# Optimization experiments

Hardware: AMD Instinct MI355X
Metric: run time of the kernel (lower is better)

Reference implementation:

```python
import jax, jax.numpy as jnp
import numpy as np
import math

B, S, D, H, L, DFF, NHEADS_OUT = 2, 1024, 1024, 16, 4, 4096, 3
DK = D // H
LN_EPS = 1e-5


def setup_inputs() -> dict:
    key = jax.random.key(0)
    ks = jax.random.split(key, 16)
    w = lambda k, shp: jax.random.normal(k, shp, dtype=jnp.float32) * 0.02
    return {
        "src": jax.random.normal(ks[0], (B, S, 1), dtype=jnp.float32),
        "emb_w": w(ks[1], (1, D)), "emb_b": jnp.zeros((D,), jnp.float32),
        "pe": w(ks[2], (S, D)),
        "Wq": w(ks[3], (L, D, D)), "bq": jnp.zeros((L, D), jnp.float32),
        "Wk": w(ks[4], (L, D, D)), "bk": jnp.zeros((L, D), jnp.float32),
        "Wv": w(ks[5], (L, D, D)), "bv": jnp.zeros((L, D), jnp.float32),
        "Wo": w(ks[6], (L, D, D)), "bo": jnp.zeros((L, D), jnp.float32),
        "fc1_w": w(ks[7], (L, D, DFF)), "fc1_b": jnp.zeros((L, DFF), jnp.float32),
        "fc2_w": w(ks[8], (L, DFF, D)), "fc2_b": jnp.zeros((L, D), jnp.float32),
        "ln1_g": jnp.ones((L, D), jnp.float32), "ln1_b": jnp.zeros((L, D), jnp.float32),
        "ln2_g": jnp.ones((L, D), jnp.float32), "ln2_b": jnp.zeros((L, D), jnp.float32),
        "hw1": w(ks[9], (NHEADS_OUT, D, D)), "hb1": jnp.zeros((NHEADS_OUT, D), jnp.float32),
        "hw2": w(ks[10], (NHEADS_OUT, D, 1)), "hb2": jnp.zeros((NHEADS_OUT, 1), jnp.float32),
    }


def _layernorm(x, g, b):
    mu = jnp.mean(x, axis=-1, keepdims=True)
    var = jnp.mean((x - mu) ** 2, axis=-1, keepdims=True)
    return (x - mu) * jax.lax.rsqrt(var + LN_EPS) * g + b


def _custom_softmax(x):
    # faithful to module's custom_softmax: max (inf->0), exp, sum + 1e-9
    m = jnp.max(x, axis=-1, keepdims=True)
    m = jnp.where(jnp.isinf(m), 0.0, m)
    e = jnp.exp(x - m)
    return e / (jnp.sum(e, axis=-1, keepdims=True) + 1e-9)


def _attention(x, Wq, bq, Wk, bk, Wv, bv, Wo, bo, mask):
    b, s, d = x.shape
    split = lambda t: t.reshape(b, s, H, DK).transpose(0, 2, 1, 3)  # [B,H,S,DK]
    q = split(x @ Wq + bq)
    k = split(x @ Wk + bk)
    v = split(x @ Wv + bv)
    scores = jnp.einsum('bhqd,bhkd->bhqk', q, k) / math.sqrt(DK)
    scores = jnp.where(mask, scores, -jnp.inf)
    probs = _custom_softmax(scores)
    out = jnp.einsum('bhqk,bhkd->bhqd', probs, v)
    out = out.transpose(0, 2, 1, 3).reshape(b, s, d)
    return out @ Wo + bo


def reference(src, emb_w, emb_b, pe, Wq, bq, Wk, bk, Wv, bv, Wo, bo,
              fc1_w, fc1_b, fc2_w, fc2_b, ln1_g, ln1_b, ln2_g, ln2_b,
              hw1, hb1, hw2, hb2):
    s = src.shape[1]
    mask = jnp.tril(jnp.ones((s, s), dtype=bool))[None, None]  # causal [1,1,S,S]
    x = src @ emb_w + emb_b          # [B,S,D]
    x = x + pe[:s]                   # learned positional encoding
    for l in range(L):
        attn = _attention(x, Wq[l], bq[l], Wk[l], bk[l], Wv[l], bv[l], Wo[l], bo[l], mask)
        h = _layernorm(x + attn, ln1_g[l], ln1_b[l])
        x = h + attn                 # quirk in original forward_step
        ff = jax.nn.relu(jax.nn.relu(x @ fc1_w[l] + fc1_b[l]) @ fc2_w[l] + fc2_b[l])
        h2 = _layernorm(x + ff, ln2_g[l], ln2_b[l])
        x = h2 + ff                  # quirk in original forward_step
    # output_size independent 2-layer heads, each -> scalar; stack on last dim
    hid = jax.nn.relu(jnp.einsum('bsd,odf->bsof', x, hw1) + hb1[None, None])  # [B,S,3,D]
    out = jnp.einsum('bsof,ofe->bsoe', hid, hw2) + hb2[None, None]            # [B,S,3,1]
    return out[..., 0]               # [B,S,3]
```

## Files before the change

kernel.cpp:

```cpp
#include <hip/hip_runtime.h>
#include <hip/hip_bf16.h>


#define BB 2
#define SS 1024
#define DD 1024
#define HH 16
#define LL 4
#define DFFC 4096
#define DKC 64

typedef __attribute__((ext_vector_type(8))) short short8;
typedef __attribute__((ext_vector_type(4))) float f32x4;

#define GLD16(gptr, ldsptr) \
    __builtin_amdgcn_global_load_lds( \
        (const __attribute__((address_space(1))) unsigned int*)(gptr), \
        (__attribute__((address_space(3))) unsigned int*)(ldsptr), 16, 0, 0)

__device__ __forceinline__ float ldin(const void* p, long long i, int isbf) {
    if (isbf) {
        unsigned int u = ((unsigned int)((const unsigned short*)p)[i]) << 16;
        return __uint_as_float(u);
    }
    return ((const float*)p)[i];
}
__device__ __forceinline__ unsigned short f2bf(float f) {
    unsigned int u = __float_as_uint(f);
    return (unsigned short)((u + 0x7FFFu + ((u >> 16) & 1u)) >> 16);
}
__device__ __forceinline__ float bf2f(unsigned short h) {
    return __uint_as_float(((unsigned int)h) << 16);
}

__global__ void k_detect(const void* __restrict__ ln1g, int* __restrict__ flag) {
    unsigned int w = *(const unsigned int*)ln1g;
    *flag = (w == 0x3F800000u) ? 0 : 1;
}

__global__ void k_embed(const void* __restrict__ src, const void* __restrict__ emb_w,
                        const void* __restrict__ emb_b, const void* __restrict__ pe,
                        float* __restrict__ x, unsigned short* __restrict__ xb,
                        const int* __restrict__ flag) {
    int row = blockIdx.x;
    int s = row & (SS - 1);
    int isbf = *flag;
    float sv = ldin(src, row, isbf);
    for (int d = threadIdx.x; d < DD; d += 256) {
        float v = sv * ldin(emb_w, d, isbf) + ldin(emb_b, d, isbf) + ldin(pe, (long long)s * DD + d, isbf);
        x[(long long)row * DD + d] = v;
        xb[(long long)row * DD + d] = f2bf(v);
    }
}

struct TSlot { const void* src; long long off; int ldw; int nrows; int ncols; long long dstoff; };
struct TArgs { TSlot s[4]; };

__global__ __launch_bounds__(256) void k_wtrans(TArgs ta, unsigned short* __restrict__ dst,
                                                const int* __restrict__ flag) {
    TSlot sl = ta.s[blockIdx.z];
    if (!sl.src) return;
    int k0 = blockIdx.x * 64, n0 = blockIdx.y * 64;
    if (k0 >= sl.nrows || n0 >= sl.ncols) return;
    int isbf = *flag;
    __shared__ float tile[64][65];
    int tid = threadIdx.x;
    int c = tid & 63, rg = tid >> 6;
    #pragma unroll
    for (int i = 0; i < 16; i++) {
        int kr = rg * 16 + i;
        tile[kr][c] = ldin(sl.src, sl.off + (long long)(k0 + kr) * sl.ldw + n0 + c, isbf);
    }
    __syncthreads();
    int nr = tid >> 2, kc = (tid & 3) * 16;
    unsigned short* dp = dst + sl.dstoff + (long long)(n0 + nr) * sl.nrows + k0 + kc;
    unsigned short h[16];
    #pragma unroll
    for (int j = 0; j < 16; j++) h[j] = f2bf(tile[kc + j][nr]);
    uint4 u0, u1;
    u0.x = h[0] | (h[1] << 16);  u0.y = h[2] | (h[3] << 16);
    u0.z = h[4] | (h[5] << 16);  u0.w = h[6] | (h[7] << 16);
    u1.x = h[8] | (h[9] << 16);  u1.y = h[10] | (h[11] << 16);
    u1.z = h[12] | (h[13] << 16); u1.w = h[14] | (h[15] << 16);
    *(uint4*)&dp[0] = u0;
    *(uint4*)&dp[8] = u1;
}

template <int MF, int NF>
__global__ __launch_bounds__(256) void k_gemm_mfma(
    const unsigned short* __restrict__ A, int lda,
    const unsigned short* __restrict__ Wt,
    const void* b0, const void* b1, const void* b2,
    long long o0, long long o1, long long o2,
    float* __restrict__ C, int ldc,
    unsigned short* __restrict__ Cb, int ldcb,
    int K, int act, int accum, const int* __restrict__ flag)
{
    const int BM = 32 * MF;
    const int BN = 32 * NF;
    __shared__ __align__(16) unsigned short As[2][BM * 32];
    __shared__ __align__(16) unsigned short Bs[2][BN * 32];
    int bflag = *flag;
    int tid = threadIdx.x;
    int wave = tid >> 6, lane = tid & 63, quad = lane >> 4, l16 = lane & 15;
    int wm = (wave & 1) * 16 * MF, wn = (wave >> 1) * 16 * NF;
    int bm = blockIdx.y * BM, bn = blockIdx.x * BN;
    int srow = lane >> 2;
    int scol = (lane & 3) * 8;

    f32x4 acc[MF][NF];
    #pragma unroll
    for (int i = 0; i < MF; i++)
        #pragma unroll
        for (int j = 0; j < NF; j++) acc[i][j] = (f32x4){0.f, 0.f, 0.f, 0.f};

    const unsigned short* Abase = A + (size_t)bm * lda;

    auto stage = [&](int k0, int p) {
        #pragma unroll
        for (int i = 0; i < MF / 2; i++) {
            int s = wave * (MF / 2) + i;
            GLD16(Abase + (size_t)(s * 16 + srow) * lda + k0 + scol, &As[p][(s * 16) * 32]);
        }
        #pragma unroll
        for (int i = 0; i < NF / 2; i++) {
            int s = wave * (NF / 2) + i;
            GLD16(Wt + (size_t)(bn + s * 16 + srow) * K + k0 + scol, &Bs[p][(s * 16) * 32]);
        }
    };

    int nk = K >> 5;
    stage(0, 0);
    for (int it = 0; it < nk; it++) {
        int p = it & 1;
        __syncthreads();
        if (it + 1 < nk) stage((it + 1) << 5, p ^ 1);

        short8 af[MF], bf[NF];
        #pragma unroll
        for (int mi = 0; mi < MF; mi++)
            af[mi] = *(const short8*)&As[p][(wm + mi * 16 + l16) * 32 + quad * 8];
        #pragma unroll
        for (int ni = 0; ni < NF; ni++)
            bf[ni] = *(const short8*)&Bs[p][(wn + ni * 16 + l16) * 32 + quad * 8];
        #pragma unroll
        for (int mi = 0; mi < MF; mi++)
            #pragma unroll
            for (int ni = 0; ni < NF; ni++)
                acc[mi][ni] = __builtin_amdgcn_mfma_f32_16x16x32_bf16(af[mi], bf[ni], acc[mi][ni], 0, 0, 0);
    }

    #pragma unroll
    for (int ni = 0; ni < NF; ni++) {
        int cn = bn + wn + ni * 16 + l16;
        float bval = 0.0f;
        if (b0) {
            int sel = cn >> 10;
            const void* bp = (sel == 0) ? b0 : (sel == 1) ? b1 : b2;
            long long oo = (sel == 0) ? o0 : (sel == 1) ? o1 : o2;
            bval = ldin(bp, oo + (cn - (sel << 10)), bflag);
        }
        #pragma unroll
        for (int mi = 0; mi < MF; mi++) {
            #pragma unroll
            for (int rr = 0; rr < 4; rr++) {
                int cm = bm + wm + mi * 16 + quad * 4 + rr;
                float v = acc[mi][ni][rr] + bval;
                if (accum) v += C[(size_t)cm * ldc + cn];
                if (act) v = fmaxf(v, 0.0f);
                if (C) C[(size_t)cm * ldc + cn] = v;
                if (Cb) Cb[(size_t)cm * ldcb + cn] = f2bf(v);
            }
        }
    }
}

__global__ __launch_bounds__(256) void k_attn(const unsigned short* __restrict__ qkv,
                                              float* __restrict__ part0,
                                              float* __restrict__ part1,
                                              float* __restrict__ rs)
{
    __shared__ __align__(16) unsigned short Vt[2][64 * 72];
    __shared__ __align__(16) unsigned short Ps[4][16 * 72];

    int tid = threadIdx.x;
    int wave = tid >> 6, lane = tid & 63, quad = lane >> 4, l16 = lane & 15;
    int qt = 15 - blockIdx.x;
    int bh = blockIdx.y;
    int split = blockIdx.z;
    int b = bh >> 4, h = bh & 15;
    int q0 = qt * 64;
    int qbase = q0 + wave * 16;

    int nk = qt + 1;
    int half = (nk + 1) >> 1;
    int kt0 = split ? half : 0;
    int kt1 = split ? nk : half;

    const unsigned short* qrow = qkv + (size_t)(b * SS + qbase + l16) * 3072 + h * DKC;
    short8 aq0 = *(const short8*)(qrow + quad * 8);
    short8 aq1 = *(const short8*)(qrow + 32 + quad * 8);

    f32x4 oacc[4];
    #pragma unroll
    for (int nt = 0; nt < 4; nt++) oacc[nt] = (f32x4){0.f, 0.f, 0.f, 0.f};
    float rsum[4] = {0.f, 0.f, 0.f, 0.f};

    int kp = tid & 31;
    int vc = (tid >> 5) * 8;
    unsigned short* pw = &Ps[wave][0];

    auto stageV = [&](int k0, int p) {
        const unsigned short* v0 = qkv + (size_t)(b * SS + k0 + 2 * kp) * 3072 + 2048 + h * DKC + vc;
        short8 s0 = *(const short8*)v0;
        short8 s1 = *(const short8*)(v0 + 3072);
        unsigned int* vt32 = (unsigned int*)&Vt[p][0];
        #pragma unroll
        for (int i = 0; i < 8; i++) {
            unsigned int pr = ((unsigned int)(unsigned short)s0[i]) |
                              (((unsigned int)(unsigned short)s1[i]) << 16);
            vt32[(vc + i) * 36 + kp] = pr;
        }
    };

    if (kt0 < kt1) stageV(kt0 * 64, 0);
    for (int kt = kt0; kt < kt1; kt++) {
        int k0 = kt * 64;
        int p = (kt - kt0) & 1;
        __syncthreads();
        if (kt + 1 < kt1) stageV(k0 + 64, p ^ 1);

        short8 bk0[4], bk1[4];
        #pragma unroll
        for (int nt = 0; nt < 4; nt++) {
            const unsigned short* krow =
                qkv + (size_t)(b * SS + k0 + nt * 16 + l16) * 3072 + 1024 + h * DKC + quad * 8;
            bk0[nt] = *(const short8*)(krow);
            bk1[nt] = *(const short8*)(krow + 32);
        }

        f32x4 sacc[4];
        #pragma unroll
        for (int nt = 0; nt < 4; nt++) {
            sacc[nt] = (f32x4){0.f, 0.f, 0.f, 0.f};
            sacc[nt] = __builtin_amdgcn_mfma_f32_16x16x32_bf16(aq0, bk0[nt], sacc[nt], 0, 0, 0);
            sacc[nt] = __builtin_amdgcn_mfma_f32_16x16x32_bf16(aq1, bk1[nt], sacc[nt], 0, 0, 0);
        }

        #pragma unroll
        for (int nt = 0; nt < 4; nt++) {
            int key = k0 + nt * 16 + l16;
            #pragma unroll
            for (int rr = 0; rr < 4; rr++) {
                float pv = __expf(sacc[nt][rr] * 0.125f);
                if (key > qbase + quad * 4 + rr) pv = 0.0f;
                rsum[rr] += pv;
                pw[(quad * 4 + rr) * 72 + nt * 16 + l16] = f2bf(pv);
            }
        }

        short8 ap0 = *(const short8*)&pw[l16 * 72 + quad * 8];
        short8 ap1 = *(const short8*)&pw[l16 * 72 + 32 + quad * 8];
        #pragma unroll
        for (int nt = 0; nt < 4; nt++) {
            short8 bv0 = *(const short8*)&Vt[p][(nt * 16 + l16) * 72 + quad * 8];
            short8 bv1 = *(const short8*)&Vt[p][(nt * 16 + l16) * 72 + 32 + quad * 8];
            oacc[nt] = __builtin_amdgcn_mfma_f32_16x16x32_bf16(ap0, bv0, oacc[nt], 0, 0, 0);
            oacc[nt] = __builtin_amdgcn_mfma_f32_16x16x32_bf16(ap1, bv1, oacc[nt], 0, 0, 0);
        }
    }

    #pragma unroll
    for (int m = 1; m < 16; m <<= 1) {
        #pragma unroll
        for (int rr = 0; rr < 4; rr++)
            rsum[rr] += __shfl_xor(rsum[rr], m, 64);
    }
    float* part = split ? part1 : part0;
    #pragma unroll
    for (int rr = 0; rr < 4; rr++) {
        int q = qbase + quad * 4 + rr;
        size_t obase = (size_t)(b * SS + q) * 1024 + h * DKC;
        #pragma unroll
        for (int nt = 0; nt < 4; nt++)
            part[obase + nt * 16 + l16] = oacc[nt][rr];
        if (l16 == 0)
            rs[(((size_t)split * 2 + b) * 16 + h) * 1024 + q] = rsum[rr];
    }
}

__global__ __launch_bounds__(256) void k_comb(const float* __restrict__ p0,
                                              const float* __restrict__ p1,
                                              const float* __restrict__ rs,
                                              unsigned short* __restrict__ qkv)
{
    int row = blockIdx.x;
    int b = row >> 10, q = row & 1023;
    int tid = threadIdx.x;
    int col = tid * 4;
    int h = col >> 6;
    float r0 = rs[(((size_t)0 + b) * 16 + h) * 1024 + q];
    float r1 = rs[(((size_t)2 + b) * 16 + h) * 1024 + q];
    float inv = 1.0f / (r0 + r1 + 1e-9f);
    size_t base = (size_t)row * 1024 + col;
    float4 a = *(const float4*)(p0 + base);
    float4 c = *(const float4*)(p1 + base);
    unsigned short* dst = qkv + (size_t)row * 3072 + col;
    uint2 w;
    w.x = f2bf((a.x + c.x) * inv) | (f2bf((a.y + c.y) * inv) << 16);
    w.y = f2bf((a.z + c.z) * inv) | (f2bf((a.w + c.w) * inv) << 16);
    *(uint2*)dst = w;
}

__global__ __launch_bounds__(256) void k_addlnadd(float* __restrict__ x, const float* __restrict__ t,
                                                  const void* __restrict__ g, long long goff,
                                                  const void* __restrict__ bta, long long boff,
                                                  unsigned short* __restrict__ xb,
                                                  const int* __restrict__ flag)
{
    int row = blockIdx.x;
    int tid = threadIdx.x;
    int isbf = *flag;
    __shared__ float red[256];
    long long base = (long long)row * DD;

    float yv[4], tv[4];
    float lsum = 0.0f;
    #pragma unroll
    for (int i = 0; i < 4; i++) {
        int d = tid + i * 256;
        tv[i] = t[base + d];
        yv[i] = x[base + d] + tv[i];
        lsum += yv[i];
    }
    red[tid] = lsum;
    __syncthreads();
    for (int s = 128; s > 0; s >>= 1) {
        if (tid < s) red[tid] += red[tid + s];
        __syncthreads();
    }
    float mu = red[0] * (1.0f / DD);
    __syncthreads();

    float lv = 0.0f;
    #pragma unroll
    for (int i = 0; i < 4; i++) {
        float dl = yv[i] - mu;
        lv += dl * dl;
    }
    red[tid] = lv;
    __syncthreads();
    for (int s = 128; s > 0; s >>= 1) {
        if (tid < s) red[tid] += red[tid + s];
        __syncthreads();
    }
    float rs = rsqrtf(red[0] * (1.0f / DD) + 1e-5f);

    #pragma unroll
    for (int i = 0; i < 4; i++) {
        int d = tid + i * 256;
        float nrm = (yv[i] - mu) * rs * ldin(g, goff + d, isbf) + ldin(bta, boff + d, isbf);
        float xo = nrm + tv[i];
        x[base + d] = xo;
        xb[base + d] = f2bf(xo);
    }
}

__global__ __launch_bounds__(256) void k_head(const unsigned short* __restrict__ hid,
                                              const void* __restrict__ hw2,
                                              const void* __restrict__ hb2,
                                              void* __restrict__ out,
                                              const int* __restrict__ flag)
{
    int row = blockIdx.x;
    int o = blockIdx.y;
    int tid = threadIdx.x;
    int isbf = *flag;
    __shared__ float red[256];
    long long base = (long long)row * 3072 + o * 1024;
    float acc = 0.0f;
    for (int f = tid; f < DD; f += 256)
        acc += bf2f(hid[base + f]) * ldin(hw2, (long long)o * DD + f, isbf);
    red[tid] = acc;
    __syncthreads();
    for (int s = 128; s > 0; s >>= 1) {
        if (tid < s) red[tid] += red[tid + s];
        __syncthreads();
    }
    if (tid == 0) {
        float r = red[0] + ldin(hb2, o, isbf);
        long long idx = (long long)row * 3 + o;
        if (isbf) ((__hip_bfloat16*)out)[idx] = __float2bfloat16(r);
        else      ((float*)out)[idx] = r;
    }
}

extern "C" void kernel_launch(void* const* d_in, const int* in_sizes, int n_in,
                              void* d_out, int out_size, void* d_ws, size_t ws_size,
                              hipStream_t stream) {
    char* w = (char*)d_ws;
    int* flag = (int*)w;
    const size_t NA = (size_t)BB * SS * DD;
    float* x  = (float*)(w + 256);
    float* tb = x + NA;
    unsigned short* qkv = (unsigned short*)(tb + NA);
    unsigned short* hb  = qkv + (size_t)BB * SS * 3072;
    unsigned short* wbuf = hb + (size_t)BB * SS * 2048;
    unsigned short* xb = wbuf + 4 * (size_t)DD * DD;
    float* rsbuf = (float*)(xb + NA);

    const long long MM = (long long)DD * DD;
    dim3 blk(256);
    TSlot z = {nullptr, 0, 1, 0, 0, 0};

    k_detect<<<1, 1, 0, stream>>>(d_in[16], flag);
    k_embed<<<BB * SS, blk, 0, stream>>>(d_in[0], d_in[1], d_in[2], d_in[3], x, xb, flag);

    for (int l = 0; l < LL; l++) {
        long long wo = (long long)l * MM;
        long long bo = (long long)l * DD;
        {
            TArgs ta = {{ {d_in[4],  wo, DD, DD, DD, 0},
                          {d_in[6],  wo, DD, DD, DD, MM},
                          {d_in[8],  wo, DD, DD, DD, 2 * MM},
                          {d_in[10], wo, DD, DD, DD, 3 * MM} }};
            k_wtrans<<<dim3(16, 16, 4), blk, 0, stream>>>(ta, wbuf, flag);
        }
        k_gemm_mfma<4, 2><<<dim3(48, 16), blk, 0, stream>>>(
            xb, DD, wbuf, d_in[5], d_in[7], d_in[9], bo, bo, bo,
            nullptr, 0, qkv, 3072, DD, 0, 0, flag);
        k_attn<<<dim3(16, BB * HH, 2), blk, 0, stream>>>(qkv, tb, (float*)hb, rsbuf);
        k_comb<<<BB * SS, blk, 0, stream>>>(tb, (float*)hb, rsbuf, qkv);
        k_gemm_mfma<2, 2><<<dim3(16, 32), blk, 0, stream>>>(
            qkv, 3072, wbuf + 3 * MM, d_in[11], d_in[11], d_in[11], bo, bo, bo,
            tb, DD, nullptr, 0, DD, 0, 0, flag);
        k_addlnadd<<<BB * SS, blk, 0, stream>>>(x, tb, d_in[16], bo, d_in[17], bo, xb, flag);
        for (int c = 0; c < 2; c++) {
            long long w1off = (long long)l * DD * DFFC + (long long)c * 2048;
            long long b1off = (long long)l * DFFC + (long long)c * 2048;
            long long w2off = (long long)l * DFFC * DD + (long long)c * 2048 * DD;
            {
                TArgs ta = {{ {d_in[12], w1off, DFFC, DD, 2048, 0},
                              {d_in[14], w2off, DD, 2048, DD, 2 * MM}, z, z }};
                k_wtrans<<<dim3(32, 32, 2), blk, 0, stream>>>(ta, wbuf, flag);
            }
            k_gemm_mfma<4, 2><<<dim3(32, 16), blk, 0, stream>>>(
                xb, DD, wbuf, d_in[13], d_in[13], d_in[13], b1off, b1off + 1024, 0,
                nullptr, 0, hb, 2048, DD, 1, 0, flag);
            k_gemm_mfma<2, 2><<<dim3(16, 32), blk, 0, stream>>>(
                hb, 2048, wbuf + 2 * MM,
                (c == 1) ? d_in[15] : nullptr, d_in[15], d_in[15], bo, bo, bo,
                tb, DD, nullptr, 0, 2048, (c == 1) ? 1 : 0, c, flag);
        }
        k_addlnadd<<<BB * SS, blk, 0, stream>>>(x, tb, d_in[18], bo, d_in[19], bo, xb, flag);
    }

    {
        TArgs ta = {{ {d_in[20], 0 * MM, DD, DD, DD, 0},
                      {d_in[20], 1 * MM, DD, DD, DD, MM},
                      {d_in[20], 2 * MM, DD, DD, DD, 2 * MM}, z }};
        k_wtrans<<<dim3(16, 16, 3), blk, 0, stream>>>(ta, wbuf, flag);
    }
    k_gemm_mfma<4, 2><<<dim3(48, 16), blk, 0, stream>>>(
        xb, DD, wbuf, d_in[21], d_in[21], d_in[21], 0, 1024, 2048,
        nullptr, 0, qkv, 3072, DD, 1, 0, flag);
    k_head<<<dim3(BB * SS, 3), blk, 0, stream>>>(qkv, d_in[22], d_in[23], d_out, flag);
}
```

Measured before the change: 1.237 ms.

## Prefetch next K/V tiles into registers and remap attention blocks per XCD

The attention kernel now issues global loads for the next key tile and value tile before computing the current tile. It writes V into LDS after the PV MFMAs, so load latency overlaps with compute. The block index is also remapped so that all blocks for a given batch-head land on the same XCD, which should improve L2 reuse of K/V. This costs extra registers for the prefetched K/V fragments, which may lower occupancy.

```diff
diff --git a/kernel.cpp b/kernel.cpp
--- a/kernel.cpp
+++ b/kernel.cpp
@@ -185,9 +185,15 @@
 
     int tid = threadIdx.x;
     int wave = tid >> 6, lane = tid & 63, quad = lane >> 4, l16 = lane & 15;
-    int qt = 15 - blockIdx.x;
-    int bh = blockIdx.y;
-    int split = blockIdx.z;
+
+    int flat = blockIdx.x + (blockIdx.y << 4) + (blockIdx.z << 9);
+    int xcd = flat & 7;
+    int j = flat >> 3;
+    int bh = ((j >> 5) << 3) + xcd;
+    int r = j & 31;
+    int split = r >> 4;
+    int qt = 15 - (r & 15);
+
     int b = bh >> 4, h = bh & 15;
     int q0 = qt * 64;
     int qbase = q0 + wave * 16;
@@ -210,41 +216,56 @@
     int vc = (tid >> 5) * 8;
     unsigned short* pw = &Ps[wave][0];
 
-    auto stageV = [&](int k0, int p) {
+    short8 vs0, vs1;
+    auto loadV = [&](int k0) {
         const unsigned short* v0 = qkv + (size_t)(b * SS + k0 + 2 * kp) * 3072 + 2048 + h * DKC + vc;
-        short8 s0 = *(const short8*)v0;
-        short8 s1 = *(const short8*)(v0 + 3072);
+        vs0 = *(const short8*)v0;
+        vs1 = *(const short8*)(v0 + 3072);
+    };
+    auto writeV = [&](int p) {
         unsigned int* vt32 = (unsigned int*)&Vt[p][0];
         #pragma unroll
         for (int i = 0; i < 8; i++) {
-            unsigned int pr = ((unsigned int)(unsigned short)s0[i]) |
-                              (((unsigned int)(unsigned short)s1[i]) << 16);
+            unsigned int pr = ((unsigned int)(unsigned short)vs0[i]) |
+                              (((unsigned int)(unsigned short)vs1[i]) << 16);
             vt32[(vc + i) * 36 + kp] = pr;
         }
     };
 
-    if (kt0 < kt1) stageV(kt0 * 64, 0);
+    short8 kc0[4], kc1[4];
+    auto loadK = [&](int k0, short8 (&d0)[4], short8 (&d1)[4]) {
+        #pragma unroll
+        for (int nt = 0; nt < 4; nt++) {
+            const unsigned short* krow =
+                qkv + (size_t)(b * SS + k0 + nt * 16 + l16) * 3072 + 1024 + h * DKC + quad * 8;
+            d0[nt] = *(const short8*)(krow);
+            d1[nt] = *(const short8*)(krow + 32);
+        }
+    };
+
+    if (kt0 < kt1) {
+        loadV(kt0 * 64);
+        loadK(kt0 * 64, kc0, kc1);
+        writeV(0);
+    }
     for (int kt = kt0; kt < kt1; kt++) {
         int k0 = kt * 64;
         int p = (kt - kt0) & 1;
         __syncthreads();
-        if (kt + 1 < kt1) stageV(k0 + 64, p ^ 1);
-
-        short8 bk0[4], bk1[4];
-        #pragma unroll
-        for (int nt = 0; nt < 4; nt++) {
-            const unsigned short* krow =
-                qkv + (size_t)(b * SS + k0 + nt * 16 + l16) * 3072 + 1024 + h * DKC + quad * 8;
-            bk0[nt] = *(const short8*)(krow);
-            bk1[nt] = *(const short8*)(krow + 32);
+
+        short8 kn0[4], kn1[4];
+        int havenext = (kt + 1 < kt1);
+        if (havenext) {
+            loadV(k0 + 64);
+            loadK(k0 + 64, kn0, kn1);
         }
 
         f32x4 sacc[4];
         #pragma unroll
         for (int nt = 0; nt < 4; nt++) {
             sacc[nt] = (f32x4){0.f, 0.f, 0.f, 0.f};
-            sacc[nt] = __builtin_amdgcn_mfma_f32_16x16x32_bf16(aq0, bk0[nt], sacc[nt], 0, 0, 0);
-            sacc[nt] = __builtin_amdgcn_mfma_f32_16x16x32_bf16(aq1, bk1[nt], sacc[nt], 0, 0, 0);
+            sacc[nt] = __builtin_amdgcn_mfma_f32_16x16x32_bf16(aq0, kc0[nt], sacc[nt], 0, 0, 0);
+            sacc[nt] = __builtin_amdgcn_mfma_f32_16x16x32_bf16(aq1, kc1[nt], sacc[nt], 0, 0, 0);
         }
 
         #pragma unroll
@@ -267,6 +288,12 @@
             short8 bv1 = *(const short8*)&Vt[p][(nt * 16 + l16) * 72 + 32 + quad * 8];
             oacc[nt] = __builtin_amdgcn_mfma_f32_16x16x32_bf16(ap0, bv0, oacc[nt], 0, 0, 0);
             oacc[nt] = __builtin_amdgcn_mfma_f32_16x16x32_bf16(ap1, bv1, oacc[nt], 0, 0, 0);
+        }
+
+        if (havenext) {
+            writeV(p ^ 1);
+            #pragma unroll
+            for (int nt = 0; nt < 4; nt++) { kc0[nt] = kn0[nt]; kc1[nt] = kn1[nt]; }
         }
     }
 
```

After: 1.200 ms. 1.03x faster.
